# Performance work log

Measured on AMD Instinct MI355X. Metric: run time of the kernel, lower is better.

Reference implementation:

```python
import jax, jax.numpy as jnp
import numpy as np

B, S_LEN, H, NH, NT, NL, I = 8, 2048, 768, 12, 32, 9, 3072
SPAN = 64
NSP = S_LEN // SPAN
TAG_RATE = 2
DH = H // NH
EPS = 1e-12


def rope(x):
    # interleaved-pair rotary position embedding, x: [B, L, H]
    L = x.shape[1]
    half = x.shape[2] // 2
    inv = 1.0 / (10000.0 ** (jnp.arange(half, dtype=jnp.float32) / half))
    ang = jnp.arange(L, dtype=jnp.float32)[:, None] * inv[None, :]  # [L, half]
    sin, cos = jnp.sin(ang), jnp.cos(ang)
    x2 = x.reshape(x.shape[0], L, half, 2)
    xe, xo = x2[..., 0], x2[..., 1]
    return jnp.stack([xe * cos - xo * sin, xe * sin + xo * cos], axis=-1).reshape(x.shape)


def layernorm(x, g, b):
    m = jnp.mean(x, axis=-1, keepdims=True)
    v = jnp.mean((x - m) ** 2, axis=-1, keepdims=True)
    return (x - m) * jax.lax.rsqrt(v + EPS) * g + b


def mha(q_in, kv_in, Wqkv, bqkv, Wo, bo):
    # torch nn.MultiheadAttention math (eval), batched over leading span axis
    Wq, Wk, Wv = jnp.split(Wqkv, 3, axis=0)
    bq, bk, bv = jnp.split(bqkv, 3)
    def heads(x, W, b):
        return (x @ W.T + b).reshape(x.shape[0], x.shape[1], NH, DH)
    q = heads(q_in, Wq, bq)
    k = heads(kv_in, Wk, bk)
    v = heads(kv_in, Wv, bv)
    scores = jnp.einsum('nqhd,nkhd->nhqk', q, k) * (1.0 / DH ** 0.5)
    a = jax.nn.softmax(scores, axis=-1)
    o = jnp.einsum('nhqk,nkhd->nqhd', a, v).reshape(q_in.shape[0], q_in.shape[1], H)
    return o @ Wo.T + bo


def setup_inputs() -> dict:
    key = jax.random.key(0)
    ks = jax.random.split(key, 16)
    p = lambda i, shape: (0.02 * jax.random.normal(ks[i], shape)).astype(jnp.float32)
    inp = {}
    inp['word_embedding'] = jax.random.normal(ks[0], (B, S_LEN, H), dtype=jnp.float32)
    # fixed-length, non-overlapping spans covering the sequence
    inp['span_starts'] = jnp.broadcast_to(jnp.arange(NSP, dtype=jnp.int32) * SPAN, (B, NSP))
    inp['span_tags'] = jax.random.randint(ks[1], (B, NSP), 0, NT)
    inp['tag_emb'] = p(2, (NT, H))
    inp['sa_Wqkv'] = p(3, (3 * H, H)); inp['sa_bqkv'] = jnp.zeros((3 * H,), jnp.float32)
    inp['sa_Wo'] = p(4, (H, H)); inp['sa_bo'] = jnp.zeros((H,), jnp.float32)
    inp['at_Wqkv'] = p(5, (3 * H, H)); inp['at_bqkv'] = jnp.zeros((3 * H,), jnp.float32)
    inp['at_Wo'] = p(6, (H, H)); inp['at_bo'] = jnp.zeros((H,), jnp.float32)
    inp['an_g'] = jnp.ones((H,), jnp.float32); inp['an_b'] = jnp.zeros((H,), jnp.float32)
    inp['W1'] = p(7, (I, H)); inp['b1'] = jnp.zeros((I,), jnp.float32)
    inp['W2'] = p(8, (H, I)); inp['b2'] = jnp.zeros((H,), jnp.float32)
    inp['fn_g'] = jnp.ones((H,), jnp.float32); inp['fn_b'] = jnp.zeros((H,), jnp.float32)
    inp['Wout'] = p(9, (NL, H)); inp['bout'] = jnp.zeros((NL,), jnp.float32)
    return inp


def reference(word_embedding, span_starts, span_tags, tag_emb,
              sa_Wqkv, sa_bqkv, sa_Wo, sa_bo,
              at_Wqkv, at_bqkv, at_Wo, at_bo,
              an_g, an_b, W1, b1, W2, b2, fn_g, fn_b, Wout, bout):
    raw = word_embedding  # hidden dropout p=0 (eval) -> identity
    xe = rope(word_embedding)
    # pack all spans: [B, NSP*SPAN] token positions
    pos = (span_starts[..., None] + jnp.arange(SPAN)).reshape(B, NSP * SPAN)
    spans = jnp.take_along_axis(xe, pos[..., None], axis=1).reshape(B * NSP, SPAN, H)
    # if_add_a_self_attention: X += self_attention(X, X, X)
    X = spans + mha(spans, spans, sa_Wqkv, sa_bqkv, sa_Wo, sa_bo)
    # enumerate_mode == 'self_attention': prepend tag embedding token, self-attend, drop it
    tagv = tag_emb[span_tags.reshape(-1)][:, None, :]  # [B*NSP, 1, H]
    qkv = jnp.concatenate([tagv, X], axis=1)           # [B*NSP, SPAN+1, H]
    res = mha(qkv, qkv, at_Wqkv, at_bqkv, at_Wo, at_bo)[:, 1:, :]
    # scatter-add results back into the full sequence
    taged = jnp.zeros_like(word_embedding).at[jnp.arange(B)[:, None], pos].add(
        res.reshape(B, NSP * SPAN, H))
    # if_merge_by_add branch
    out_emb = layernorm(raw + taged * TAG_RATE, an_g, an_b)
    ff = jax.nn.relu(out_emb @ W1.T + b1) @ W2.T + b2
    out = layernorm(ff + out_emb, fn_g, fn_b)
    return out @ Wout.T + bout
```

## Files before the change

kernel.cpp:

```cpp
#include <hip/hip_runtime.h>


typedef __attribute__((ext_vector_type(8))) short short8;
typedef __attribute__((ext_vector_type(4))) float f32x4;

typedef const __attribute__((address_space(1))) unsigned int* gas1_t;
typedef __attribute__((address_space(3))) unsigned int* las3_t;

#define DEVI static __device__ __forceinline__
#define VMCNT(n) asm volatile("s_waitcnt vmcnt(" #n ")" ::: "memory")

DEVI void gload_lds16(const void* g, void* l){
  __builtin_amdgcn_global_load_lds((gas1_t)g, (las3_t)l, 16, 0, 0);
}

DEVI unsigned short f2bf(float f){
  union { float f; unsigned u; } v; v.f = f;
  unsigned u = v.u;
  return (unsigned short)((u + 0x7fffu + ((u >> 16) & 1u)) >> 16);
}
DEVI float bf2f(unsigned short h){
  union { unsigned u; float f; } v; v.u = ((unsigned)h) << 16; return v.f;
}

__global__ void k_ropetab(float2* __restrict__ tab){
  int idx = blockIdx.x * 256 + threadIdx.x;
  if (idx >= 2048 * 384) return;
  int l = idx / 384, i = idx % 384;
  float inv = __expf(-(float)i * (9.210340371976184f / 384.0f));
  float ang = (float)l * inv;
  tab[idx] = make_float2(cosf(ang), sinf(ang));
}

__global__ void k_f2bf(const float* __restrict__ src, unsigned short* __restrict__ dst, int n){
  int i = blockIdx.x * 256 + threadIdx.x;
  if (i * 4 >= n) return;
  float4 v = *(const float4*)(src + (size_t)i * 4);
  ushort4 o;
  o.x = f2bf(v.x); o.y = f2bf(v.y); o.z = f2bf(v.z); o.w = f2bf(v.w);
  *(ushort4*)(dst + (size_t)i * 4) = o;
}

__global__ void k_gather_rope(const float* __restrict__ we, const int* __restrict__ starts,
                              const float2* __restrict__ tab, unsigned short* __restrict__ spans){
  int idx = blockIdx.x * 256 + threadIdx.x;
  int r  = idx / 192;
  int c4 = idx % 192;
  int span = r >> 6, s = r & 63;
  int b = span >> 5;
  int l = starts[span] + s;
  float4 x = *(const float4*)(we + ((size_t)b * 2048 + l) * 768 + c4 * 4);
  int i0 = c4 * 2;
  float2 cs0 = tab[l * 384 + i0];
  float2 cs1 = tab[l * 384 + i0 + 1];
  ushort4 o;
  o.x = f2bf(x.x * cs0.x - x.y * cs0.y);
  o.y = f2bf(x.x * cs0.y + x.y * cs0.x);
  o.z = f2bf(x.z * cs1.x - x.w * cs1.y);
  o.w = f2bf(x.z * cs1.y + x.w * cs1.x);
  *(ushort4*)(spans + (size_t)r * 768 + c4 * 4) = o;
}

__global__ void k_fill_tag(const float* __restrict__ tag_emb, const int* __restrict__ tags,
                           unsigned short* __restrict__ at_in){
  int span = blockIdx.x;
  int tag = tags[span];
  const float* src = tag_emb + (size_t)tag * 768;
  unsigned short* dst = at_in + (size_t)span * 65 * 768;
  for (int j = threadIdx.x; j < 768; j += 256) dst[j] = f2bf(src[j]);
}

template<int EPI>
__global__ __launch_bounds__(512, 2)
void k_gemm256(const unsigned short* __restrict__ A, const unsigned short* __restrict__ Bw,
               const float* __restrict__ bias, void* __restrict__ outp,
               const unsigned short* __restrict__ resid, int M, int N, int K, int nbx)
{
  __shared__ unsigned short Asl[4 * 256 * 32];
  __shared__ unsigned short Bsl[4 * 256 * 32];
  const int t0 = threadIdx.x;
  const int w = t0 >> 6, lane = t0 & 63;
  const int g = lane >> 4, li = lane & 15;
  const int wm = w >> 2, wn = w & 3;

  const int nwg = gridDim.x;
  const int bid = blockIdx.x;
  const int q = nwg >> 3, r8 = nwg & 7;
  const int xcd = bid & 7, off = bid >> 3;
  const int swz = (xcd < r8 ? xcd * (q + 1) : r8 * (q + 1) + (xcd - r8) * q) + off;
  const int m0 = (swz / nbx) * 256, n0 = (swz % nbx) * 256;

  const int srow = lane >> 2;
  const int sgc = (((lane & 3) ^ ((lane >> 3) & 3)) << 3);
  const int cs = ((g ^ ((li >> 1) & 3)) << 3);

  f32x4 acc[8][4];
  #pragma unroll
  for (int i = 0; i < 8; i++)
    #pragma unroll
    for (int j = 0; j < 4; j++) acc[i][j] = f32x4{0.f, 0.f, 0.f, 0.f};

  const int KT = K >> 5;

  #define STAGE(t_, s_) do { \
    const unsigned short* ga0 = A  + (size_t)(m0 +       w*16 + srow) * K + (t_)*32 + sgc; \
    const unsigned short* ga1 = A  + (size_t)(m0 + 128 + w*16 + srow) * K + (t_)*32 + sgc; \
    const unsigned short* gb0 = Bw + (size_t)(n0 +       w*16 + srow) * K + (t_)*32 + sgc; \
    const unsigned short* gb1 = Bw + (size_t)(n0 + 128 + w*16 + srow) * K + (t_)*32 + sgc; \
    gload_lds16(ga0, Asl + (s_)*8192 + (      w*16)*32); \
    gload_lds16(ga1, Asl + (s_)*8192 + (128 + w*16)*32); \
    gload_lds16(gb0, Bsl + (s_)*8192 + (      w*16)*32); \
    gload_lds16(gb1, Bsl + (s_)*8192 + (128 + w*16)*32); \
  } while(0)

  STAGE(0, 0);
  STAGE(1, 1);
  VMCNT(4);
  __builtin_amdgcn_s_barrier();

  for (int t = 0; t < KT; ++t){
    const int slot = t & 3;
    const unsigned short* As = Asl + slot * 8192;
    const unsigned short* Bs = Bsl + slot * 8192;

    short8 af[8], bfr[4];
    #pragma unroll
    for (int m = 0; m < 8; m++)
      af[m] = *(const short8*)(As + (wm * 128 + m * 16 + li) * 32 + cs);
    #pragma unroll
    for (int n = 0; n < 4; n++)
      bfr[n] = *(const short8*)(Bs + (wn * 64 + n * 16 + li) * 32 + cs);

    if (t + 2 < KT) STAGE(t + 2, (t + 2) & 3);

    #pragma unroll
    for (int m = 0; m < 8; m++)
      #pragma unroll
      for (int n = 0; n < 4; n++)
        acc[m][n] = __builtin_amdgcn_mfma_f32_16x16x32_bf16(af[m], bfr[n], acc[m][n], 0, 0, 0);

    if (t + 1 < KT){
      __builtin_amdgcn_sched_barrier(0);
      if (t + 2 < KT) { VMCNT(4); } else { VMCNT(0); }
      __builtin_amdgcn_s_barrier();
    }
  }
  #undef STAGE

  unsigned short* outb = (unsigned short*)outp;
  float* outf = (float*)outp;
  #pragma unroll
  for (int m = 0; m < 8; m++){
    const int row = m0 + wm * 128 + m * 16 + g * 4;
    #pragma unroll
    for (int n = 0; n < 4; n++){
      const int col = n0 + wn * 64 + n * 16 + li;
      const float bv = bias[col];
      #pragma unroll
      for (int r = 0; r < 4; r++){
        float v = acc[m][n][r] + bv;
        const int orow = row + r;
        if (EPI == 1) v += bf2f(resid[(size_t)orow * N + col]);
        if (EPI == 3) v = v > 0.f ? v : 0.f;
        if (EPI == 2){
          outf[(size_t)orow * N + col] = v;
        } else if (EPI == 1){
          outb[(size_t)(orow + orow / 64 + 1) * N + col] = f2bf(v);
        } else {
          outb[(size_t)orow * N + col] = f2bf(v);
        }
      }
    }
  }
}

template<int AT>
__global__ __launch_bounds__(64)
void k_attn(const unsigned short* __restrict__ qkv, unsigned short* __restrict__ outp)
{
  constexpr int Lkv  = AT ? 65 : 64;
  constexpr int qoff = AT ? 1 : 0;
  constexpr int NKF  = AT ? 5 : 4;
  constexpr int VK   = AT ? 65 : 64;
  constexpr int KKPV = AT ? 3 : 2;
  const int h = blockIdx.x;
  const int span = blockIdx.y;
  const int base = span * Lkv;
  const int lane = threadIdx.x;
  const int g = lane >> 4, li = lane & 15;

  __shared__ unsigned short P[64 * 104];
  if (AT){
    #pragma unroll
    for (int j = 0; j < 16; j++) P[lane * 104 + 80 + j] = 0;
  }

  short8 qf[4][2];
  #pragma unroll
  for (int m = 0; m < 4; m++)
    #pragma unroll
    for (int kq = 0; kq < 2; kq++)
      qf[m][kq] = *(const short8*)(qkv + (size_t)(base + qoff + m * 16 + li) * 2304 + h * 64 + kq * 32 + g * 8);

  f32x4 sc[4][NKF];
  #pragma unroll
  for (int m = 0; m < 4; m++)
    #pragma unroll
    for (int n = 0; n < NKF; n++) sc[m][n] = f32x4{0.f, 0.f, 0.f, 0.f};

  #pragma unroll
  for (int kq = 0; kq < 2; kq++){
    #pragma unroll
    for (int n = 0; n < NKF; n++){
      int krow = n * 16 + li; if (krow >= Lkv) krow = Lkv - 1;
      short8 kf = *(const short8*)(qkv + (size_t)(base + krow) * 2304 + 768 + h * 64 + kq * 32 + g * 8);
      #pragma unroll
      for (int m = 0; m < 4; m++)
        sc[m][n] = __builtin_amdgcn_mfma_f32_16x16x32_bf16(qf[m][kq], kf, sc[m][n], 0, 0, 0);
    }
  }

  const float scale = 0.125f;
  #pragma unroll
  for (int m = 0; m < 4; m++){
    #pragma unroll
    for (int r = 0; r < 4; r++){
      float mx = -1e30f;
      #pragma unroll
      for (int n = 0; n < NKF; n++){
        float v = sc[m][n][r] * scale;
        if (n * 16 + li >= VK) v = -1e30f;
        sc[m][n][r] = v;
        mx = fmaxf(mx, v);
      }
      mx = fmaxf(mx, __shfl_xor(mx, 1, 64));
      mx = fmaxf(mx, __shfl_xor(mx, 2, 64));
      mx = fmaxf(mx, __shfl_xor(mx, 4, 64));
      mx = fmaxf(mx, __shfl_xor(mx, 8, 64));
      float sum = 0.f;
      #pragma unroll
      for (int n = 0; n < NKF; n++){
        float p = __expf(sc[m][n][r] - mx);
        sc[m][n][r] = p;
        sum += p;
      }
      sum += __shfl_xor(sum, 1, 64);
      sum += __shfl_xor(sum, 2, 64);
      sum += __shfl_xor(sum, 4, 64);
      sum += __shfl_xor(sum, 8, 64);
      const float inv = 1.f / sum;
      const int prow = m * 16 + g * 4 + r;
      #pragma unroll
      for (int n = 0; n < NKF; n++)
        P[prow * 104 + n * 16 + li] = f2bf(sc[m][n][r] * inv);
    }
  }
  __syncthreads();

  f32x4 oacc[4][4];
  #pragma unroll
  for (int m = 0; m < 4; m++)
    #pragma unroll
    for (int n = 0; n < 4; n++) oacc[m][n] = f32x4{0.f, 0.f, 0.f, 0.f};

  #pragma unroll
  for (int kp = 0; kp < KKPV; kp++){
    short8 pf[4];
    #pragma unroll
    for (int m = 0; m < 4; m++)
      pf[m] = *(const short8*)(P + (m * 16 + li) * 104 + kp * 32 + g * 8);
    #pragma unroll
    for (int n = 0; n < 4; n++){
      short8 vf;
      #pragma unroll
      for (int i = 0; i < 8; i++){
        int k = kp * 32 + g * 8 + i;
        unsigned short vv = 0;
        if (k < VK) vv = qkv[(size_t)(base + k) * 2304 + 1536 + h * 64 + n * 16 + li];
        vf[i] = (short)vv;
      }
      #pragma unroll
      for (int m = 0; m < 4; m++)
        oacc[m][n] = __builtin_amdgcn_mfma_f32_16x16x32_bf16(pf[m], vf, oacc[m][n], 0, 0, 0);
    }
  }

  #pragma unroll
  for (int m = 0; m < 4; m++)
    #pragma unroll
    for (int n = 0; n < 4; n++)
      #pragma unroll
      for (int r = 0; r < 4; r++){
        int q = m * 16 + g * 4 + r;
        outp[(size_t)(span * 64 + q) * 768 + h * 64 + n * 16 + li] = f2bf(oacc[m][n][r]);
      }
}

__global__ __launch_bounds__(256)
void k_ln1(const float* __restrict__ raw, const float* __restrict__ res,
           const int* __restrict__ starts, const float* __restrict__ gg,
           const float* __restrict__ bb, unsigned short* __restrict__ oe16)
{
  int wave = threadIdx.x >> 6, lane = threadIdx.x & 63;
  int r = blockIdx.x * 4 + wave;
  int span = r >> 6, s = r & 63;
  int b = span >> 5;
  int l = starts[span] + s;
  const float* rp = raw + ((size_t)b * 2048 + l) * 768;
  const float* qp = res + (size_t)r * 768;
  float x[12];
  float sum = 0.f;
  #pragma unroll
  for (int j = 0; j < 12; j++){
    int c = lane + j * 64;
    x[j] = rp[c] + 2.f * qp[c];
    sum += x[j];
  }
  #pragma unroll
  for (int o = 1; o < 64; o <<= 1) sum += __shfl_xor(sum, o, 64);
  float mean = sum * (1.f / 768.f);
  float vs = 0.f;
  #pragma unroll
  for (int j = 0; j < 12; j++){ float d = x[j] - mean; vs += d * d; }
  #pragma unroll
  for (int o = 1; o < 64; o <<= 1) vs += __shfl_xor(vs, o, 64);
  float rstd = rsqrtf(vs * (1.f / 768.f) + 1e-12f);
  size_t ob = ((size_t)b * 2048 + l) * 768;
  #pragma unroll
  for (int j = 0; j < 12; j++){
    int c = lane + j * 64;
    float y = (x[j] - mean) * rstd * gg[c] + bb[c];
    oe16[ob + c] = f2bf(y);
  }
}

__global__ __launch_bounds__(256)
void k_ln2_out(const unsigned short* __restrict__ ff2, const unsigned short* __restrict__ oe,
               const float* __restrict__ gg, const float* __restrict__ bb,
               const float* __restrict__ Wout, const float* __restrict__ bout,
               float* __restrict__ out)
{
  int wave = threadIdx.x >> 6, lane = threadIdx.x & 63;
  int t = blockIdx.x * 4 + wave;
  const unsigned short* fp = ff2 + (size_t)t * 768;
  const unsigned short* ep = oe  + (size_t)t * 768;
  float x[12];
  float sum = 0.f;
  #pragma unroll
  for (int j = 0; j < 12; j++){
    int c = lane + j * 64;
    x[j] = bf2f(fp[c]) + bf2f(ep[c]);
    sum += x[j];
  }
  #pragma unroll
  for (int o = 1; o < 64; o <<= 1) sum += __shfl_xor(sum, o, 64);
  float mean = sum * (1.f / 768.f);
  float vs = 0.f;
  #pragma unroll
  for (int j = 0; j < 12; j++){ float d = x[j] - mean; vs += d * d; }
  #pragma unroll
  for (int o = 1; o < 64; o <<= 1) vs += __shfl_xor(vs, o, 64);
  float rstd = rsqrtf(vs * (1.f / 768.f) + 1e-12f);
  #pragma unroll
  for (int j = 0; j < 12; j++){
    int c = lane + j * 64;
    x[j] = (x[j] - mean) * rstd * gg[c] + bb[c];
  }
  for (int n = 0; n < 9; n++){
    float p = 0.f;
    #pragma unroll
    for (int j = 0; j < 12; j++){
      int c = lane + j * 64;
      p += x[j] * Wout[n * 768 + c];
    }
    #pragma unroll
    for (int o = 1; o < 64; o <<= 1) p += __shfl_xor(p, o, 64);
    if (lane == 0) out[(size_t)t * 9 + n] = p + bout[n];
  }
}

extern "C" void kernel_launch(void* const* d_in, const int* in_sizes, int n_in,
                              void* d_out, int out_size, void* d_ws, size_t ws_size,
                              hipStream_t stream)
{
  const float* we      = (const float*)d_in[0];
  const int*   starts  = (const int*)d_in[1];
  const int*   tags    = (const int*)d_in[2];
  const float* tag_emb = (const float*)d_in[3];
  const float* sa_Wqkv = (const float*)d_in[4];
  const float* sa_bqkv = (const float*)d_in[5];
  const float* sa_Wo   = (const float*)d_in[6];
  const float* sa_bo   = (const float*)d_in[7];
  const float* at_Wqkv = (const float*)d_in[8];
  const float* at_bqkv = (const float*)d_in[9];
  const float* at_Wo   = (const float*)d_in[10];
  const float* at_bo   = (const float*)d_in[11];
  const float* an_g    = (const float*)d_in[12];
  const float* an_b    = (const float*)d_in[13];
  const float* W1      = (const float*)d_in[14];
  const float* b1      = (const float*)d_in[15];
  const float* W2      = (const float*)d_in[16];
  const float* b2      = (const float*)d_in[17];
  const float* fn_g    = (const float*)d_in[18];
  const float* fn_b    = (const float*)d_in[19];
  const float* Wout    = (const float*)d_in[20];
  const float* bout    = (const float*)d_in[21];
  float* out = (float*)d_out;
  char* ws = (char*)d_ws;

  unsigned short* spans   = (unsigned short*)(ws + 0);
  unsigned short* at_in   = (unsigned short*)(ws + 25165824);
  unsigned short* attno   = (unsigned short*)(ws + 50724864);
  unsigned short* qkv     = (unsigned short*)(ws + 75890688);
  float2*         ropetab = (float2*)(ws + 75890688);
  float*          resf    = (float*)(ws + 75890688);
  unsigned short* oe16    = (unsigned short*)(ws + 0);
  unsigned short* ff1     = (unsigned short*)(ws + 25165824);
  unsigned short* ff2     = (unsigned short*)(ws + 125829120);
  unsigned short* wb      = (unsigned short*)(ws + 152567808);
  unsigned short* sa_Wqkv_b = wb;
  unsigned short* sa_Wo_b   = sa_Wqkv_b + 2304 * 768;
  unsigned short* at_Wqkv_b = sa_Wo_b   + 768 * 768;
  unsigned short* at_Wo_b   = at_Wqkv_b + 2304 * 768;
  unsigned short* W1_b      = at_Wo_b   + 768 * 768;
  unsigned short* W2_b      = W1_b      + 3072 * 768;

  k_ropetab<<<3072, 256, 0, stream>>>(ropetab);
  k_f2bf<<<1728, 256, 0, stream>>>(sa_Wqkv, sa_Wqkv_b, 2304 * 768);
  k_f2bf<<< 576, 256, 0, stream>>>(sa_Wo,   sa_Wo_b,    768 * 768);
  k_f2bf<<<1728, 256, 0, stream>>>(at_Wqkv, at_Wqkv_b, 2304 * 768);
  k_f2bf<<< 576, 256, 0, stream>>>(at_Wo,   at_Wo_b,    768 * 768);
  k_f2bf<<<2304, 256, 0, stream>>>(W1,      W1_b,      3072 * 768);
  k_f2bf<<<2304, 256, 0, stream>>>(W2,      W2_b,       768 * 3072);
  k_gather_rope<<<12288, 256, 0, stream>>>(we, starts, ropetab, spans);

  k_gemm256<0><<<576, 512, 0, stream>>>(spans, sa_Wqkv_b, sa_bqkv, qkv, nullptr, 16384, 2304, 768, 9);
  k_attn<0><<<dim3(12, 256), 64, 0, stream>>>(qkv, attno);
  k_fill_tag<<<256, 256, 0, stream>>>(tag_emb, tags, at_in);
  k_gemm256<1><<<192, 512, 0, stream>>>(attno, sa_Wo_b, sa_bo, at_in, spans, 16384, 768, 768, 3);
  k_gemm256<0><<<585, 512, 0, stream>>>(at_in, at_Wqkv_b, at_bqkv, qkv, nullptr, 16640, 2304, 768, 9);
  k_attn<1><<<dim3(12, 256), 64, 0, stream>>>(qkv, attno);
  k_gemm256<2><<<192, 512, 0, stream>>>(attno, at_Wo_b, at_bo, resf, nullptr, 16384, 768, 768, 3);
  k_ln1<<<4096, 256, 0, stream>>>(we, resf, starts, an_g, an_b, oe16);
  k_gemm256<3><<<768, 512, 0, stream>>>(oe16, W1_b, b1, ff1, nullptr, 16384, 3072, 768, 12);
  k_gemm256<0><<<192, 512, 0, stream>>>(ff1, W2_b, b2, ff2, nullptr, 16384, 768, 3072, 3);
  k_ln2_out<<<4096, 256, 0, stream>>>(ff2, oe16, fn_g, fn_b, Wout, bout, out);
}
```

Before: 500.6 us.

## Template GEMM tile size, deepen prefetch to three stages, raise MFMA priority

The GEMM kernel is templated on the M/N tile size. The three N=768 GEMMs now use 128x256 tiles, giving 384 workgroups instead of 192 so the 256 CUs are better filled. The LDS prefetch pipeline goes from two to three tiles in flight, with vmcnt waits adjusted per tile size, and s_setprio brackets the MFMA loop. Smaller tiles cost more operand reloads per output, and deeper prefetch keeps the same 4-slot LDS buffer with tighter slot reuse.

Result: slower. 547.3 us (+9.3%).

```diff
diff --git a/kernel.cpp b/kernel.cpp
--- a/kernel.cpp
+++ b/kernel.cpp
@@ -8,10 +8,17 @@
 typedef __attribute__((address_space(3))) unsigned int* las3_t;
 
 #define DEVI static __device__ __forceinline__
-#define VMCNT(n) asm volatile("s_waitcnt vmcnt(" #n ")" ::: "memory")
 
 DEVI void gload_lds16(const void* g, void* l){
   __builtin_amdgcn_global_load_lds((gas1_t)g, (las3_t)l, 16, 0, 0);
+}
+
+template<int N> DEVI void vmcnt_imm(){
+  if constexpr (N == 8) asm volatile("s_waitcnt vmcnt(8)" ::: "memory");
+  else if constexpr (N == 6) asm volatile("s_waitcnt vmcnt(6)" ::: "memory");
+  else if constexpr (N == 4) asm volatile("s_waitcnt vmcnt(4)" ::: "memory");
+  else if constexpr (N == 3) asm volatile("s_waitcnt vmcnt(3)" ::: "memory");
+  else asm volatile("s_waitcnt vmcnt(0)" ::: "memory");
 }
 
 DEVI unsigned short f2bf(float f){
@@ -70,14 +77,17 @@
   for (int j = threadIdx.x; j < 768; j += 256) dst[j] = f2bf(src[j]);
 }
 
-template<int EPI>
+template<int EPI, int TM, int TN>
 __global__ __launch_bounds__(512, 2)
 void k_gemm256(const unsigned short* __restrict__ A, const unsigned short* __restrict__ Bw,
                const float* __restrict__ bias, void* __restrict__ outp,
                const unsigned short* __restrict__ resid, int M, int N, int K, int nbx)
 {
-  __shared__ unsigned short Asl[4 * 256 * 32];
-  __shared__ unsigned short Bsl[4 * 256 * 32];
+  constexpr int WM = TM / 2, WN = TN / 4;
+  constexpr int MREP = WM / 16, NREP = WN / 16;
+  constexpr int LOADS = (TM + TN) / 128;
+  __shared__ unsigned short Asl[4 * TM * 32];
+  __shared__ unsigned short Bsl[4 * TN * 32];
   const int t0 = threadIdx.x;
   const int w = t0 >> 6, lane = t0 & 63;
   const int g = lane >> 4, li = lane & 15;
@@ -88,60 +98,69 @@
   const int q = nwg >> 3, r8 = nwg & 7;
   const int xcd = bid & 7, off = bid >> 3;
   const int swz = (xcd < r8 ? xcd * (q + 1) : r8 * (q + 1) + (xcd - r8) * q) + off;
-  const int m0 = (swz / nbx) * 256, n0 = (swz % nbx) * 256;
+  const int m0 = (swz / nbx) * TM, n0 = (swz % nbx) * TN;
 
   const int srow = lane >> 2;
   const int sgc = (((lane & 3) ^ ((lane >> 3) & 3)) << 3);
   const int cs = ((g ^ ((li >> 1) & 3)) << 3);
 
-  f32x4 acc[8][4];
-  #pragma unroll
-  for (int i = 0; i < 8; i++)
-    #pragma unroll
-    for (int j = 0; j < 4; j++) acc[i][j] = f32x4{0.f, 0.f, 0.f, 0.f};
+  f32x4 acc[MREP][NREP];
+  #pragma unroll
+  for (int i = 0; i < MREP; i++)
+    #pragma unroll
+    for (int j = 0; j < NREP; j++) acc[i][j] = f32x4{0.f, 0.f, 0.f, 0.f};
 
   const int KT = K >> 5;
 
   #define STAGE(t_, s_) do { \
     const unsigned short* ga0 = A  + (size_t)(m0 +       w*16 + srow) * K + (t_)*32 + sgc; \
-    const unsigned short* ga1 = A  + (size_t)(m0 + 128 + w*16 + srow) * K + (t_)*32 + sgc; \
+    gload_lds16(ga0, Asl + (s_)*TM*32 + (      w*16)*32); \
+    if constexpr (TM == 256) { \
+      const unsigned short* ga1 = A  + (size_t)(m0 + 128 + w*16 + srow) * K + (t_)*32 + sgc; \
+      gload_lds16(ga1, Asl + (s_)*TM*32 + (128 + w*16)*32); \
+    } \
     const unsigned short* gb0 = Bw + (size_t)(n0 +       w*16 + srow) * K + (t_)*32 + sgc; \
-    const unsigned short* gb1 = Bw + (size_t)(n0 + 128 + w*16 + srow) * K + (t_)*32 + sgc; \
-    gload_lds16(ga0, Asl + (s_)*8192 + (      w*16)*32); \
-    gload_lds16(ga1, Asl + (s_)*8192 + (128 + w*16)*32); \
-    gload_lds16(gb0, Bsl + (s_)*8192 + (      w*16)*32); \
-    gload_lds16(gb1, Bsl + (s_)*8192 + (128 + w*16)*32); \
+    gload_lds16(gb0, Bsl + (s_)*TN*32 + (      w*16)*32); \
+    if constexpr (TN == 256) { \
+      const unsigned short* gb1 = Bw + (size_t)(n0 + 128 + w*16 + srow) * K + (t_)*32 + sgc; \
+      gload_lds16(gb1, Bsl + (s_)*TN*32 + (128 + w*16)*32); \
+    } \
   } while(0)
 
   STAGE(0, 0);
   STAGE(1, 1);
-  VMCNT(4);
+  STAGE(2, 2);
+  vmcnt_imm<2 * LOADS>();
   __builtin_amdgcn_s_barrier();
 
   for (int t = 0; t < KT; ++t){
     const int slot = t & 3;
-    const unsigned short* As = Asl + slot * 8192;
-    const unsigned short* Bs = Bsl + slot * 8192;
-
-    short8 af[8], bfr[4];
-    #pragma unroll
-    for (int m = 0; m < 8; m++)
-      af[m] = *(const short8*)(As + (wm * 128 + m * 16 + li) * 32 + cs);
-    #pragma unroll
-    for (int n = 0; n < 4; n++)
-      bfr[n] = *(const short8*)(Bs + (wn * 64 + n * 16 + li) * 32 + cs);
-
-    if (t + 2 < KT) STAGE(t + 2, (t + 2) & 3);
-
-    #pragma unroll
-    for (int m = 0; m < 8; m++)
-      #pragma unroll
-      for (int n = 0; n < 4; n++)
+    const unsigned short* As = Asl + slot * TM * 32;
+    const unsigned short* Bs = Bsl + slot * TN * 32;
+
+    short8 af[MREP], bfr[NREP];
+    #pragma unroll
+    for (int m = 0; m < MREP; m++)
+      af[m] = *(const short8*)(As + (wm * WM + m * 16 + li) * 32 + cs);
+    #pragma unroll
+    for (int n = 0; n < NREP; n++)
+      bfr[n] = *(const short8*)(Bs + (wn * WN + n * 16 + li) * 32 + cs);
+
+    if (t + 3 < KT) STAGE(t + 3, (t + 3) & 3);
+
+    __builtin_amdgcn_s_setprio(1);
+    #pragma unroll
+    for (int m = 0; m < MREP; m++)
+      #pragma unroll
+      for (int n = 0; n < NREP; n++)
         acc[m][n] = __builtin_amdgcn_mfma_f32_16x16x32_bf16(af[m], bfr[n], acc[m][n], 0, 0, 0);
+    __builtin_amdgcn_s_setprio(0);
 
     if (t + 1 < KT){
       __builtin_amdgcn_sched_barrier(0);
-      if (t + 2 < KT) { VMCNT(4); } else { VMCNT(0); }
+      if (t + 3 < KT)      vmcnt_imm<2 * LOADS>();
+      else if (t + 2 < KT) vmcnt_imm<LOADS>();
+      else                 vmcnt_imm<0>();
       __builtin_amdgcn_s_barrier();
     }
   }
@@ -150,11 +169,11 @@
   unsigned short* outb = (unsigned short*)outp;
   float* outf = (float*)outp;
   #pragma unroll
-  for (int m = 0; m < 8; m++){
-    const int row = m0 + wm * 128 + m * 16 + g * 4;
-    #pragma unroll
-    for (int n = 0; n < 4; n++){
-      const int col = n0 + wn * 64 + n * 16 + li;
+  for (int m = 0; m < MREP; m++){
+    const int row = m0 + wm * WM + m * 16 + g * 4;
+    #pragma unroll
+    for (int n = 0; n < NREP; n++){
+      const int col = n0 + wn * WN + n * 16 + li;
       const float bv = bias[col];
       #pragma unroll
       for (int r = 0; r < 4; r++){
@@ -434,15 +453,15 @@
   k_f2bf<<<2304, 256, 0, stream>>>(W2,      W2_b,       768 * 3072);
   k_gather_rope<<<12288, 256, 0, stream>>>(we, starts, ropetab, spans);
 
-  k_gemm256<0><<<576, 512, 0, stream>>>(spans, sa_Wqkv_b, sa_bqkv, qkv, nullptr, 16384, 2304, 768, 9);
+  k_gemm256<0,256,256><<<576, 512, 0, stream>>>(spans, sa_Wqkv_b, sa_bqkv, qkv, nullptr, 16384, 2304, 768, 9);
   k_attn<0><<<dim3(12, 256), 64, 0, stream>>>(qkv, attno);
   k_fill_tag<<<256, 256, 0, stream>>>(tag_emb, tags, at_in);
-  k_gemm256<1><<<192, 512, 0, stream>>>(attno, sa_Wo_b, sa_bo, at_in, spans, 16384, 768, 768, 3);
-  k_gemm256<0><<<585, 512, 0, stream>>>(at_in, at_Wqkv_b, at_bqkv, qkv, nullptr, 16640, 2304, 768, 9);
+  k_gemm256<1,128,256><<<384, 512, 0, stream>>>(attno, sa_Wo_b, sa_bo, at_in, spans, 16384, 768, 768, 3);
+  k_gemm256<0,256,256><<<585, 512, 0, stream>>>(at_in, at_Wqkv_b, at_bqkv, qkv, nullptr, 16640, 2304, 768, 9);
   k_attn<1><<<dim3(12, 256), 64, 0, stream>>>(qkv, attno);
-  k_gemm256<2><<<192, 512, 0, stream>>>(attno, at_Wo_b, at_bo, resf, nullptr, 16384, 768, 768, 3);
+  k_gemm256<2,128,256><<<384, 512, 0, stream>>>(attno, at_Wo_b, at_bo, resf, nullptr, 16384, 768, 768, 3);
   k_ln1<<<4096, 256, 0, stream>>>(we, resf, starts, an_g, an_b, oe16);
-  k_gemm256<3><<<768, 512, 0, stream>>>(oe16, W1_b, b1, ff1, nullptr, 16384, 3072, 768, 12);
-  k_gemm256<0><<<192, 512, 0, stream>>>(ff1, W2_b, b2, ff2, nullptr, 16384, 768, 3072, 3);
+  k_gemm256<3,256,256><<<768, 512, 0, stream>>>(oe16, W1_b, b1, ff1, nullptr, 16384, 3072, 768, 12);
+  k_gemm256<0,128,256><<<384, 512, 0, stream>>>(ff1, W2_b, b2, ff2, nullptr, 16384, 768, 3072, 3);
   k_ln2_out<<<4096, 256, 0, stream>>>(ff2, oe16, fn_g, fn_b, Wout, bout, out);
 }
```
